# Kernel optimization log

Measured on AMD Instinct MI355X. Metric: run time of the kernel, lower is better.

## Reference

```python
import jax, jax.numpy as jnp
import numpy as np

N, E, D, H, LAYERS = 50000, 800000, 128, 8, 2
LRELU_ALPHA = 0.2


def _seg_softmax(logits, seg, n):
    # numerically stable softmax over edges grouped by destination node
    m = jax.ops.segment_max(logits, seg, num_segments=n)
    z = jnp.exp(logits - m[seg])
    s = jax.ops.segment_sum(z, seg, num_segments=n)
    return z / jnp.maximum(s[seg], 1e-16)


def _gat_layer(x, src, dst, W, a_src, a_dst, concat):
    # W: [H, Fin, F'], a_src/a_dst: [H, F']
    n = x.shape[0]
    outs = []
    for h in range(W.shape[0]):  # loop over heads to bound peak memory
        Wh = x @ W[h]                              # [N, F']
        es = Wh @ a_src[h]                         # [N]
        ed = Wh @ a_dst[h]                         # [N]
        e = jax.nn.leaky_relu(es[src] + ed[dst], LRELU_ALPHA)  # [E]
        att = _seg_softmax(e, dst, n)              # [E]
        out = jax.ops.segment_sum(att[:, None] * Wh[src], dst, num_segments=n)
        outs.append(out)
    if concat:
        return jax.nn.elu(jnp.concatenate(outs, axis=-1))  # [N, H*F']
    return jnp.mean(jnp.stack(outs, axis=0), axis=0)        # [N, F']


def _rel_gcn_layer(x, src, dst, w, W):
    # weighted-adjacency GCN with row (in-degree) normalization + ReLU
    n = x.shape[0]
    deg = jax.ops.segment_sum(w, dst, num_segments=n)
    norm = w / jnp.maximum(deg[dst], 1e-16)        # [E]
    h = x @ W                                      # [N, Dout]
    agg = jax.ops.segment_sum(norm[:, None] * h[src], dst, num_segments=n)
    return jax.nn.relu(agg)


def setup_inputs() -> dict:
    key = jax.random.key(0)
    ks = jax.random.split(key, 12)
    s = 1.0 / np.sqrt(D)
    return {
        "x": jax.random.normal(ks[0], (N, D), dtype=jnp.float32),
        "edge_index": jax.random.randint(ks[1], (2, E), 0, N, dtype=jnp.int64),
        "edge_weight": jax.random.uniform(ks[2], (E,), dtype=jnp.float32),
        "gat_W0": jax.random.normal(ks[3], (H, D, D // H), dtype=jnp.float32) * s,
        "gat_a0_src": jax.random.normal(ks[4], (H, D // H), dtype=jnp.float32) * s,
        "gat_a0_dst": jax.random.normal(ks[5], (H, D // H), dtype=jnp.float32) * s,
        "gat_W1": jax.random.normal(ks[6], (H, D, D), dtype=jnp.float32) * s,
        "gat_a1_src": jax.random.normal(ks[7], (H, D), dtype=jnp.float32) * s,
        "gat_a1_dst": jax.random.normal(ks[8], (H, D), dtype=jnp.float32) * s,
        "gcn_W0": jax.random.normal(ks[9], (D, D), dtype=jnp.float32) * s,
        "gcn_W1": jax.random.normal(ks[10], (D, D), dtype=jnp.float32) * s,
    }


def reference(x, edge_index, edge_weight, gat_W0, gat_a0_src, gat_a0_dst,
              gat_W1, gat_a1_src, gat_a1_dst, gcn_W0, gcn_W1):
    src, dst = edge_index[0], edge_index[1]
    gat_params = [(gat_W0, gat_a0_src, gat_a0_dst), (gat_W1, gat_a1_src, gat_a1_dst)]
    gcn_params = [gcn_W0, gcn_W1]
    x1, x2 = x, x  # dropout is identity in eval mode
    for i in range(LAYERS):
        W, a_s, a_d = gat_params[i]
        x1 = _gat_layer(x1, src, dst, W, a_s, a_d, concat=(i != LAYERS - 1))
        x2 = _rel_gcn_layer(x2, src, dst, edge_weight, gcn_params[i])
    # cat along new last dim then MaxPool1d(2) == elementwise max of branches
    return jnp.maximum(x1, x2)
```

## Files before the change

kernel.cpp:

```cpp
#include <hip/hip_runtime.h>

#define LRELU_ALPHA 0.2f

typedef __attribute__((ext_vector_type(8))) short short8;
typedef __attribute__((ext_vector_type(4))) float float4v;
typedef __attribute__((ext_vector_type(2))) float f32x2;

__device__ __forceinline__ unsigned short f2bf(float f) {
  union { float f; unsigned u; } x; x.f = f;
  unsigned r = (x.u + 0x7fff + ((x.u >> 16) & 1)) >> 16;
  return (unsigned short)r;
}
__device__ __forceinline__ float bflo(unsigned u) {
  union { unsigned u; float f; } x; x.u = u << 16; return x.f;
}
__device__ __forceinline__ float bfhi(unsigned u) {
  union { unsigned u; float f; } x; x.u = u & 0xffff0000u; return x.f;
}
__device__ __forceinline__ f32x2 bfpair(unsigned u) {
  return (f32x2){bflo(u), bfhi(u)};
}
__device__ __forceinline__ unsigned packbf(float a, float b) {
  return (unsigned)f2bf(a) | ((unsigned)f2bf(b) << 16);
}


__global__ __launch_bounds__(256) void k_count(const int* __restrict__ dst,
                                               int* __restrict__ cnt, int E) {
  int e = blockIdx.x * 256 + threadIdx.x;
  if (e < E) atomicAdd(&cnt[dst[e]], 1);
}

__global__ __launch_bounds__(1024) void k_scan1(const int* __restrict__ cnt,
                                                int* __restrict__ lscan,
                                                int* __restrict__ bsum, int N) {
  __shared__ int sm[1024];
  int t = threadIdx.x;
  int base = blockIdx.x * 1024;
  int v = (base + t < N) ? cnt[base + t] : 0;
  sm[t] = v;
  __syncthreads();
  for (int off = 1; off < 1024; off <<= 1) {
    int x = (t >= off) ? sm[t - off] : 0;
    __syncthreads();
    sm[t] += x;
    __syncthreads();
  }
  if (base + t < N) lscan[base + t] = sm[t] - v;
  if (t == 1023) bsum[blockIdx.x] = sm[1023];
}

__global__ __launch_bounds__(64) void k_scan2(int* __restrict__ bsum,
                                              int* __restrict__ rowptrN, int nb) {
  int t = threadIdx.x;
  int v = (t < nb) ? bsum[t] : 0;
  int orig = v;
  for (int off = 1; off < 64; off <<= 1) {
    int y = __shfl_up(v, off, 64);
    if (t >= off) v += y;
  }
  if (t < nb) bsum[t] = v - orig;
  if (t == 63) *rowptrN = v;
}

__global__ __launch_bounds__(1024) void k_scan3(int* __restrict__ rowptr,
                                                int* __restrict__ cur,
                                                const int* __restrict__ bsum, int N) {
  int i = blockIdx.x * 1024 + threadIdx.x;
  if (i < N) {
    int v = rowptr[i] + bsum[blockIdx.x];
    rowptr[i] = v;
    cur[i] = v;
  }
}

__global__ __launch_bounds__(256) void k_scatter(const int* __restrict__ src,
                                                 const int* __restrict__ dst,
                                                 const float* __restrict__ w,
                                                 const float* __restrict__ logit0,
                                                 int* __restrict__ cur,
                                                 uint2* __restrict__ edata,
                                                 unsigned short* __restrict__ pedge,
                                                 int E) {
  int base = (blockIdx.x * 256 + threadIdx.x) * 4;
  if (base >= E) return;
  int n = E - base; if (n > 4) n = 4;
  int ss[4], dd[4]; float ww[4];
  if (n == 4) {
    int4 s4 = *(const int4*)(src + base);
    int4 d4 = *(const int4*)(dst + base);
    float4 w4 = *(const float4*)(w + base);
    ss[0] = s4.x; ss[1] = s4.y; ss[2] = s4.z; ss[3] = s4.w;
    dd[0] = d4.x; dd[1] = d4.y; dd[2] = d4.z; dd[3] = d4.w;
    ww[0] = w4.x; ww[1] = w4.y; ww[2] = w4.z; ww[3] = w4.w;
  } else {
    for (int i = 0; i < n; ++i) { ss[i] = src[base + i]; dd[i] = dst[base + i]; ww[i] = w[base + i]; }
  }
  int pp[4];
#pragma unroll
  for (int i = 0; i < 4; ++i)
    if (i < n) pp[i] = atomicAdd(&cur[dd[i]], 1);
#pragma unroll
  for (int i = 0; i < 4; ++i) {
    if (i >= n) break;
    int s = ss[i], d = dd[i], p = pp[i];
    edata[p] = make_uint2((unsigned)s, __float_as_uint(ww[i]));
    float4 es0 = *(const float4*)(logit0 + (size_t)s * 16);
    float4 es1 = *(const float4*)(logit0 + (size_t)s * 16 + 4);
    float4 ed0 = *(const float4*)(logit0 + (size_t)d * 16 + 8);
    float4 ed1 = *(const float4*)(logit0 + (size_t)d * 16 + 12);
    float lg[8] = {es0.x + ed0.x, es0.y + ed0.y, es0.z + ed0.z, es0.w + ed0.w,
                   es1.x + ed1.x, es1.y + ed1.y, es1.z + ed1.z, es1.w + ed1.w};
    unsigned short o[8];
#pragma unroll
    for (int h = 0; h < 8; ++h) {
      float v = lg[h] > 0.f ? lg[h] : LRELU_ALPHA * lg[h];
      o[h] = f2bf(__expf(fminf(v, 80.f)));
    }
    ushort4 q0 = {o[0], o[1], o[2], o[3]};
    ushort4 q1 = {o[4], o[5], o[6], o[7]};
    *(ushort4*)(pedge + (size_t)p * 8) = q0;
    *(ushort4*)(pedge + (size_t)p * 8 + 4) = q1;
  }
}

__global__ __launch_bounds__(256) void k_pack(const float* __restrict__ W0,
                                              const float* __restrict__ a0s,
                                              const float* __restrict__ a0d,
                                              const float* __restrict__ W1,
                                              const float* __restrict__ a1s,
                                              const float* __restrict__ a1d,
                                              const float* __restrict__ gw0,
                                              const float* __restrict__ gw1,
                                              unsigned short* __restrict__ W0catT,
                                              float* __restrict__ logitW,
                                              unsigned short* __restrict__ gw1T,
                                              unsigned short* __restrict__ va1T,
                                              unsigned short* __restrict__ WstackT) {
  int idx = blockIdx.x * 256 + threadIdx.x;
  if (idx < 32768) {
    int n = idx >> 7, k = idx & 127;
    float v;
    if (n < 128) {
      int h = n >> 4, f = n & 15;
      v = W0[h * 2048 + k * 16 + f];
    } else {
      v = gw0[k * 128 + (n - 128)];
    }
    W0catT[idx] = f2bf(v);
  } else if (idx < 34816) {
    int j = idx - 32768;
    int k = j >> 4, c = j & 15;
    int h = (c < 8) ? c : c - 8;
    const float* a = (c < 8) ? a0s : a0d;
    float s = 0.f;
    for (int f = 0; f < 16; ++f) s += W0[h * 2048 + k * 16 + f] * a[h * 16 + f];
    logitW[j] = s;
  } else if (idx < 51200) {
    int j = idx - 34816;
    int n = j >> 7, k = j & 127;
    gw1T[j] = f2bf(gw1[k * 128 + n]);
  } else if (idx < 53248) {
    int j = idx - 51200;
    int c = j >> 7, k = j & 127;
    int h = c & 7;
    const float* a = (c < 8) ? a1s : a1d;
    float s = 0.f;
    for (int f = 0; f < 128; ++f) s += W1[h * 16384 + k * 128 + f] * a[h * 128 + f];
    va1T[j] = f2bf(s);
  } else if (idx < 184320) {
    int j = idx - 53248;
    int n = j >> 10, kk = j & 1023;
    int h = kk >> 7, k = kk & 127;
    WstackT[j] = f2bf(W1[h * 16384 + k * 128 + n] * 0.125f);
  }
}

__global__ __launch_bounds__(256) void k_prep(const float* __restrict__ x,
                                              const float* __restrict__ logitW,
                                              unsigned short* __restrict__ xb,
                                              float* __restrict__ logit0, int N) {
  __shared__ float sm[16][132];
  __shared__ float sw[2048];
  int t = threadIdx.x;
  int base = blockIdx.x * 16;
  int r = t >> 4, cc = (t & 15) * 8;
  const float* xr = x + (size_t)(base + r) * 128 + cc;
  float4 v0 = *(const float4*)xr;
  float4 v1 = *(const float4*)(xr + 4);
  ushort4 o0 = {f2bf(v0.x), f2bf(v0.y), f2bf(v0.z), f2bf(v0.w)};
  ushort4 o1 = {f2bf(v1.x), f2bf(v1.y), f2bf(v1.z), f2bf(v1.w)};
  *(ushort4*)(xb + (size_t)(base + r) * 128 + cc) = o0;
  *(ushort4*)(xb + (size_t)(base + r) * 128 + cc + 4) = o1;
  *(float4*)&sm[r][cc] = v0;
  *(float4*)&sm[r][cc + 4] = v1;
  *(float4*)&sw[t * 8] = *(const float4*)(logitW + t * 8);
  *(float4*)&sw[t * 8 + 4] = *(const float4*)(logitW + t * 8 + 4);
  __syncthreads();
  int c = t & 15;
  float acc = 0.f;
#pragma unroll
  for (int k = 0; k < 128; ++k) acc += sm[r][k] * sw[k * 16 + c];
  logit0[(size_t)(base + r) * 16 + c] = acc;
}

__global__ __launch_bounds__(256) void k_pedge(const float* __restrict__ logits,
                                               const uint2* __restrict__ edata,
                                               const int* __restrict__ rowptr,
                                               unsigned short* __restrict__ pedge,
                                               float* __restrict__ linv, int N) {
  int wave = threadIdx.x >> 6, lane = threadIdx.x & 63;
  int d = blockIdx.x * 4 + wave;
  if (d >= N) return;
  int j8 = lane >> 3, h = lane & 7;
  float edv = logits[(size_t)d * 16 + 8 + h];
  int beg = rowptr[d], end = rowptr[d + 1];
  float lsum = 0.f;
  for (int ii = beg + j8; ii < end; ii += 8) {
    unsigned s = edata[ii].x;
    float es = logits[(size_t)s * 16 + h];
    float lg = es + edv;
    lg = lg > 0.f ? lg : LRELU_ALPHA * lg;
    float p = __expf(fminf(lg, 80.f));
    lsum += p;
    pedge[(size_t)ii * 8 + h] = f2bf(p);
  }
  lsum += __shfl_xor(lsum, 8, 64);
  lsum += __shfl_xor(lsum, 16, 64);
  lsum += __shfl_xor(lsum, 32, 64);
  if (lane < 8) linv[(size_t)d * 8 + h] = lsum > 0.f ? 1.f / lsum : 0.f;
}

template <int NT, int OUT_BF16, int EPI>
__global__ __launch_bounds__(256) void k_mgemm(const unsigned short* __restrict__ A, int lda,
                                               const unsigned short* __restrict__ BT, int ldb,
                                               void* __restrict__ Cv, int ldc,
                                               const void* __restrict__ aux,
                                               int M, int Ncols, int K) {
  __shared__ unsigned short As[64][64];
  __shared__ unsigned short Bs[NT * 16][64];
  int tid = threadIdx.x;
  int w = tid >> 6, lane = tid & 63;
  int quad = lane >> 4, l16 = lane & 15;
  int row0 = blockIdx.x * 64;
  int c0 = blockIdx.y * (NT * 16);
  float4v acc[NT];
#pragma unroll
  for (int t = 0; t < NT; ++t) acc[t] = (float4v){0.f, 0.f, 0.f, 0.f};

  for (int k0 = 0; k0 < K; k0 += 64) {
    __syncthreads();
#pragma unroll
    for (int i = 0; i < 2; ++i) {
      int c = tid + i * 256;
      int r = c >> 3, kc = c & 7;
      uint4 v = {0u, 0u, 0u, 0u};
      int gr = row0 + r;
      if (gr < M) v = *(const uint4*)(A + (size_t)gr * lda + k0 + kc * 8);
      *(uint4*)(&As[r][(kc ^ (r & 7)) * 8]) = v;
    }
#pragma unroll
    for (int i = 0; i < (NT * 128 + 255) / 256; ++i) {
      int c = tid + i * 256;
      if (c < NT * 128) {
        int n = c >> 3, kc = c & 7;
        uint4 v = {0u, 0u, 0u, 0u};
        int gn = c0 + n;
        if (gn < Ncols) v = *(const uint4*)(BT + (size_t)gn * ldb + k0 + kc * 8);
        *(uint4*)(&Bs[n][(kc ^ (n & 7)) * 8]) = v;
      }
    }
    __syncthreads();
#pragma unroll
    for (int ks = 0; ks < 2; ++ks) {
      int m = w * 16 + l16;
      int ga = (ks * 4 + quad) ^ (m & 7);
      short8 a = *(const short8*)(&As[m][ga * 8]);
#pragma unroll
      for (int t = 0; t < NT; ++t) {
        int n = t * 16 + l16;
        int gb = (ks * 4 + quad) ^ (n & 7);
        short8 b = *(const short8*)(&Bs[n][gb * 8]);
        acc[t] = __builtin_amdgcn_mfma_f32_16x16x32_bf16(a, b, acc[t], 0, 0, 0);
      }
    }
  }
#pragma unroll
  for (int t = 0; t < NT; ++t) {
    int cc = c0 + t * 16 + l16;
    if (cc >= Ncols) continue;
#pragma unroll
    for (int i = 0; i < 4; ++i) {
      int rr = row0 + w * 16 + quad * 4 + i;
      if (rr >= M) continue;
      float v = acc[t][i];
      if (EPI == 1) {
        unsigned short us = ((const unsigned short*)aux)[(size_t)rr * ldc + cc];
        v = fmaxf(v, bflo((unsigned)us));
      }
      if (EPI == 2) {
        ((unsigned short*)Cv)[(size_t)rr * 256 + 4 * (cc >> 1) + 2 + (cc & 1)] = f2bf(v);
      } else if (EPI == 4) {
        if (cc < 128) {
          ((unsigned short*)Cv)[(size_t)rr * 128 + cc] = f2bf(v);
        } else {
          int enc = __builtin_amdgcn_cvt_pk_fp8_f32(v, v, 0, false);
          ((unsigned char*)aux)[(size_t)rr * 128 + (cc - 128)] = (unsigned char)(enc & 0xff);
        }
      } else if (OUT_BF16)
        ((unsigned short*)Cv)[(size_t)rr * ldc + cc] = f2bf(v);
      else
        ((float*)Cv)[(size_t)rr * ldc + cc] = v;
    }
  }
}

__global__ __launch_bounds__(256, 8) void k_agg0(const unsigned short* __restrict__ featg,
                                                 const unsigned char* __restrict__ featc,
                                                 const int* __restrict__ rowptr,
                                                 const uint2* __restrict__ edata,
                                                 const unsigned short* __restrict__ pedge,
                                                 unsigned short* __restrict__ x1c,
                                                 unsigned short* __restrict__ x2,
                                                 unsigned short* __restrict__ xh, int N) {
  __shared__ uint2 swl[4][64];
  __shared__ float pl[4][512];
  int wave = threadIdx.x >> 6, lane = threadIdx.x & 63;
  int head = lane >> 3;
  const unsigned* FG = (const unsigned*)featg + lane;
  const unsigned short* FC = (const unsigned short*)featc + lane;
  for (int d = blockIdx.x * 4 + wave; d < N; d += gridDim.x * 4) {
    int beg = rowptr[d], end = rowptr[d + 1], deg = end - beg;
    f32x2 aa = {0.f, 0.f}, ga = {0.f, 0.f};
    float l = 0.f, wsum = 0.f;
    for (int base = 0; base < deg; base += 64) {
      int idx = beg + base + lane;
      uint2 sv = make_uint2(0u, 0u);
      uint4 q = make_uint4(0u, 0u, 0u, 0u);
      if (idx < end) {
        sv = edata[idx];
        q = *(const uint4*)(pedge + (size_t)idx * 8);
      }
      swl[wave][lane] = sv;
      float4 pa = make_float4(bflo(q.x), bfhi(q.x), bflo(q.y), bfhi(q.y));
      float4 pb = make_float4(bflo(q.z), bfhi(q.z), bflo(q.w), bfhi(q.w));
      *(float4*)&pl[wave][lane * 8] = pa;
      *(float4*)&pl[wave][lane * 8 + 4] = pb;
      int ng = deg - base; if (ng > 64) ng = 64;
      int t = 0;
      for (; t + 4 <= ng; t += 4) {
        uint2 s0 = swl[wave][t], s1 = swl[wave][t + 1];
        uint2 s2 = swl[wave][t + 2], s3 = swl[wave][t + 3];
        unsigned g0 = FG[(size_t)s0.x * 64];
        unsigned g1 = FG[(size_t)s1.x * 64];
        unsigned g2 = FG[(size_t)s2.x * 64];
        unsigned g3 = FG[(size_t)s3.x * 64];
        unsigned c0 = (unsigned)FC[(size_t)s0.x * 64];
        unsigned c1 = (unsigned)FC[(size_t)s1.x * 64];
        unsigned c2 = (unsigned)FC[(size_t)s2.x * 64];
        unsigned c3 = (unsigned)FC[(size_t)s3.x * 64];
        float p0 = pl[wave][t * 8 + head];
        float p1 = pl[wave][t * 8 + 8 + head];
        float p2 = pl[wave][t * 8 + 16 + head];
        float p3 = pl[wave][t * 8 + 24 + head];
        float w0 = __uint_as_float(s0.y), w1 = __uint_as_float(s1.y);
        float w2 = __uint_as_float(s2.y), w3 = __uint_as_float(s3.y);
        aa += bfpair(g0) * p0; ga += __builtin_amdgcn_cvt_pk_f32_fp8(c0, false) * w0;
        l += p0; wsum += w0;
        aa += bfpair(g1) * p1; ga += __builtin_amdgcn_cvt_pk_f32_fp8(c1, false) * w1;
        l += p1; wsum += w1;
        aa += bfpair(g2) * p2; ga += __builtin_amdgcn_cvt_pk_f32_fp8(c2, false) * w2;
        l += p2; wsum += w2;
        aa += bfpair(g3) * p3; ga += __builtin_amdgcn_cvt_pk_f32_fp8(c3, false) * w3;
        l += p3; wsum += w3;
      }
      for (; t < ng; ++t) {
        uint2 s0 = swl[wave][t];
        unsigned g0 = FG[(size_t)s0.x * 64];
        unsigned c0 = (unsigned)FC[(size_t)s0.x * 64];
        float p0 = pl[wave][t * 8 + head];
        float w0 = __uint_as_float(s0.y);
        aa += bfpair(g0) * p0; ga += __builtin_amdgcn_cvt_pk_f32_fp8(c0, false) * w0;
        l += p0; wsum += w0;
      }
    }
    float inv = l > 0.f ? 1.f / l : 0.f;
    float v0 = aa.x * inv, v1 = aa.y * inv;
    v0 = v0 > 0.f ? v0 : __expf(v0) - 1.f;
    v1 = v1 > 0.f ? v1 : __expf(v1) - 1.f;
    unsigned p0 = packbf(v0, v1);
    ((unsigned*)x1c)[(size_t)d * 64 + lane] = p0;
    ((unsigned*)xh)[(size_t)d * 128 + 2 * lane] = p0;
    float ginv = 1.f / fmaxf(wsum, 1e-16f);
    ((unsigned*)x2)[(size_t)d * 64 + lane] =
        packbf(fmaxf(ga.x * ginv, 0.f), fmaxf(ga.y * ginv, 0.f));
  }
}

__global__ __launch_bounds__(256, 8) void k_agg1(const unsigned short* __restrict__ xh,
                                                 const int* __restrict__ rowptr,
                                                 const uint2* __restrict__ edata,
                                                 const unsigned short* __restrict__ pedge,
                                                 const float* __restrict__ linv,
                                                 unsigned short* __restrict__ aggbuf,
                                                 unsigned short* __restrict__ x2f, int N) {
  __shared__ uint2 swl[4][64];
  __shared__ float pl[4][512];
  int wave = threadIdx.x >> 6, lane = threadIdx.x & 63;
  const uint2* X2 = (const uint2*)xh + lane;
  for (int d = blockIdx.x * 4 + wave; d < N; d += gridDim.x * 4) {
    int beg = rowptr[d], end = rowptr[d + 1], deg = end - beg;
    f32x2 axp[8] = {};
    f32x2 gp = {0.f, 0.f};
    float wsum = 0.f;
#define EDGE1(uu, ss, tt)                                    \
  {                                                          \
    float4 pv0 = *(const float4*)&pl[wave][(tt) * 8];        \
    float4 pv1 = *(const float4*)&pl[wave][(tt) * 8 + 4];    \
    float wj = __uint_as_float((ss).y);                      \
    f32x2 xA = bfpair((uu).x), hA = bfpair((uu).y);          \
    axp[0] += xA * pv0.x; axp[1] += xA * pv0.y;              \
    axp[2] += xA * pv0.z; axp[3] += xA * pv0.w;              \
    axp[4] += xA * pv1.x; axp[5] += xA * pv1.y;              \
    axp[6] += xA * pv1.z; axp[7] += xA * pv1.w;              \
    gp += hA * wj; wsum += wj;                               \
  }
    for (int base = 0; base < deg; base += 64) {
      int idx = beg + base + lane;
      uint2 sv = make_uint2(0u, 0u);
      uint4 q = make_uint4(0u, 0u, 0u, 0u);
      if (idx < end) {
        sv = edata[idx];
        q = *(const uint4*)(pedge + (size_t)idx * 8);
      }
      swl[wave][lane] = sv;
      float4 pa = make_float4(bflo(q.x), bfhi(q.x), bflo(q.y), bfhi(q.y));
      float4 pb = make_float4(bflo(q.z), bfhi(q.z), bflo(q.w), bfhi(q.w));
      *(float4*)&pl[wave][lane * 8] = pa;
      *(float4*)&pl[wave][lane * 8 + 4] = pb;
      int ng = deg - base; if (ng > 64) ng = 64;
      int t = 0;
      for (; t + 4 <= ng; t += 4) {
        uint2 s0 = swl[wave][t], s1 = swl[wave][t + 1];
        uint2 s2 = swl[wave][t + 2], s3 = swl[wave][t + 3];
        uint2 u0 = X2[(size_t)s0.x * 64];
        uint2 u1 = X2[(size_t)s1.x * 64];
        uint2 u2 = X2[(size_t)s2.x * 64];
        uint2 u3 = X2[(size_t)s3.x * 64];
        EDGE1(u0, s0, t)
        EDGE1(u1, s1, t + 1)
        EDGE1(u2, s2, t + 2)
        EDGE1(u3, s3, t + 3)
      }
      for (; t < ng; ++t) {
        uint2 s0 = swl[wave][t];
        uint2 u0 = X2[(size_t)s0.x * 64];
        EDGE1(u0, s0, t)
      }
    }
#undef EDGE1
    float4 i0 = *(const float4*)(linv + (size_t)d * 8);
    float4 i1 = *(const float4*)(linv + (size_t)d * 8 + 4);
    unsigned* ab = (unsigned*)aggbuf + (size_t)d * 512 + lane;
    ab[0]   = packbf(axp[0].x * i0.x, axp[0].y * i0.x);
    ab[64]  = packbf(axp[1].x * i0.y, axp[1].y * i0.y);
    ab[128] = packbf(axp[2].x * i0.z, axp[2].y * i0.z);
    ab[192] = packbf(axp[3].x * i0.w, axp[3].y * i0.w);
    ab[256] = packbf(axp[4].x * i1.x, axp[4].y * i1.x);
    ab[320] = packbf(axp[5].x * i1.y, axp[5].y * i1.y);
    ab[384] = packbf(axp[6].x * i1.z, axp[6].y * i1.z);
    ab[448] = packbf(axp[7].x * i1.w, axp[7].y * i1.w);
    float ginv = 1.f / fmaxf(wsum, 1e-16f);
    ((unsigned*)x2f)[(size_t)d * 64 + lane] =
        packbf(fmaxf(gp.x * ginv, 0.f), fmaxf(gp.y * ginv, 0.f));
  }
}


extern "C" void kernel_launch(void* const* d_in, const int* in_sizes, int n_in,
                              void* d_out, int out_size, void* d_ws, size_t ws_size,
                              hipStream_t stream) {
  const float* x   = (const float*)d_in[0];
  const int*   ei  = (const int*)d_in[1];
  const float* ew  = (const float*)d_in[2];
  const float* W0  = (const float*)d_in[3];
  const float* a0s = (const float*)d_in[4];
  const float* a0d = (const float*)d_in[5];
  const float* W1  = (const float*)d_in[6];
  const float* a1s = (const float*)d_in[7];
  const float* a1d = (const float*)d_in[8];
  const float* gw0 = (const float*)d_in[9];
  const float* gw1 = (const float*)d_in[10];
  float* out = (float*)d_out;

  const int N = in_sizes[0] / 128;
  const int E = in_sizes[1] / 2;
  const int* src = ei;
  const int* dst = ei + E;

  char* p = (char*)d_ws;
  auto carve = [&](size_t bytes) {
    void* r = (void*)p;
    p += (bytes + 255) & ~(size_t)255;
    return r;
  };
  int*   cnt    = (int*)carve((size_t)N * 4);
  int*   rowptr = (int*)carve((size_t)(N + 1) * 4);
  int*   cur    = (int*)carve((size_t)N * 4);
  int*   bsum   = (int*)carve(256 * 4);
  uint2* edata  = (uint2*)carve((size_t)E * 8);
  unsigned short* W0catT  = (unsigned short*)carve(32768 * 2);
  float*          logitW  = (float*)carve(2048 * 4);
  unsigned short* gw1T    = (unsigned short*)carve(16384 * 2);
  unsigned short* va1T    = (unsigned short*)carve(2048 * 2);
  unsigned short* WstackT = (unsigned short*)carve(131072 * 2);
  unsigned short* x2   = (unsigned short*)carve((size_t)N * 128 * 2);
  float*          esed = (float*)carve((size_t)N * 16 * 4);
  unsigned short* xh   = (unsigned short*)carve((size_t)N * 256 * 2);
  unsigned short* pedge = (unsigned short*)carve((size_t)E * 8 * 2);
  float*          linv1 = (float*)carve((size_t)N * 8 * 4);
  size_t ph1 = ((size_t)N * 128 * 2 + 255) & ~(size_t)255;
  size_t ph2 = ph1 + (((size_t)N * 128 * 2 + 255) & ~(size_t)255);
  size_t ph3 = ph2 + (((size_t)N * 128 + 255) & ~(size_t)255);
  size_t ph4 = ph3 + (((size_t)N * 16 * 4 + 255) & ~(size_t)255);
  size_t scratch_sz = (size_t)N * 1024 * 2;
  if (ph4 > scratch_sz) scratch_sz = ph4;
  char* scratch = (char*)carve(scratch_sz);
  unsigned short* xb     = (unsigned short*)scratch;
  unsigned short* x1c    = (unsigned short*)scratch;
  unsigned short* featg  = (unsigned short*)(scratch + ph1);
  unsigned char*  featc  = (unsigned char*)(scratch + ph2);
  float*          logit0 = (float*)(scratch + ph3);
  unsigned short* aggbuf = (unsigned short*)scratch;
  unsigned short* x2f    = x2;

  int gE = (E + 255) / 256;
  int gE4 = ((E + 3) / 4 + 255) / 256;
  int nb = (N + 1023) / 1024;
  int gM = (N + 63) / 64;
  int gD = (N + 3) / 4;
  int gA = gD < 2048 ? gD : 2048;

  hipMemsetAsync(cnt, 0, (size_t)N * 4, stream);
  k_count<<<gE, 256, 0, stream>>>(dst, cnt, E);
  k_scan1<<<nb, 1024, 0, stream>>>(cnt, rowptr, bsum, N);
  k_scan2<<<1, 64, 0, stream>>>(bsum, rowptr + N, nb);
  k_scan3<<<nb, 1024, 0, stream>>>(rowptr, cur, bsum, N);

  k_pack<<<(184320 + 255) / 256, 256, 0, stream>>>(W0, a0s, a0d, W1, a1s, a1d, gw0,
                                                   gw1, W0catT, logitW, gw1T, va1T,
                                                   WstackT);
  k_prep<<<(N + 15) / 16, 256, 0, stream>>>(x, logitW, xb, logit0, N);

  k_scatter<<<gE4, 256, 0, stream>>>(src, dst, ew, logit0, cur, edata, pedge, E);

  k_mgemm<8, 1, 4><<<dim3(gM, 2), 256, 0, stream>>>(xb, 128, W0catT, 128, featg, 128,
                                                    featc, N, 256, 128);
  k_agg0<<<gA, 256, 0, stream>>>(featg, featc, rowptr, edata, pedge, x1c, x2, xh, N);

  k_mgemm<1, 0, 0><<<dim3(gM, 1), 256, 0, stream>>>(x1c, 128, va1T, 128, esed, 16,
                                                    nullptr, N, 16, 128);
  k_mgemm<8, 1, 2><<<dim3(gM, 1), 256, 0, stream>>>(x2, 128, gw1T, 128, xh, 256,
                                                    nullptr, N, 128, 128);

  k_pedge<<<gD, 256, 0, stream>>>(esed, edata, rowptr, pedge, linv1, N);

  k_agg1<<<gA, 256, 0, stream>>>(xh, rowptr, edata, pedge, linv1, aggbuf, x2f, N);

  k_mgemm<8, 0, 1><<<dim3(gM, 1), 256, 0, stream>>>(aggbuf, 1024, WstackT, 1024, out,
                                                    128, x2f, N, 128, 1024);
}
```

Baseline: 458.6 us.

## Compute edge attention on the fly in aggregation kernels and reorder GCN layer two

Removes the precomputed bf16 per-edge attention buffer and the separate k_pedge kernel. Both aggregation kernels now gather source logits per edge, apply leaky-ReLU and exp themselves, and reduce the softmax denominator in-register. The second GCN layer is reordered to aggregate first and then apply the weight matrix, with ReLU moved into the GEMM epilogue. This cuts edge-sized writes and reads plus one launch, at the cost of extra random logit gathers and exp work inside the aggregation loops, and an in-place GEMM on x2a.

```diff
diff --git a/kernel.cpp b/kernel.cpp
--- a/kernel.cpp
+++ b/kernel.cpp
@@ -77,11 +77,8 @@
 __global__ __launch_bounds__(256) void k_scatter(const int* __restrict__ src,
                                                  const int* __restrict__ dst,
                                                  const float* __restrict__ w,
-                                                 const float* __restrict__ logit0,
                                                  int* __restrict__ cur,
-                                                 uint2* __restrict__ edata,
-                                                 unsigned short* __restrict__ pedge,
-                                                 int E) {
+                                                 uint2* __restrict__ edata, int E) {
   int base = (blockIdx.x * 256 + threadIdx.x) * 4;
   if (base >= E) return;
   int n = E - base; if (n > 4) n = 4;
@@ -101,27 +98,8 @@
   for (int i = 0; i < 4; ++i)
     if (i < n) pp[i] = atomicAdd(&cur[dd[i]], 1);
 #pragma unroll
-  for (int i = 0; i < 4; ++i) {
-    if (i >= n) break;
-    int s = ss[i], d = dd[i], p = pp[i];
-    edata[p] = make_uint2((unsigned)s, __float_as_uint(ww[i]));
-    float4 es0 = *(const float4*)(logit0 + (size_t)s * 16);
-    float4 es1 = *(const float4*)(logit0 + (size_t)s * 16 + 4);
-    float4 ed0 = *(const float4*)(logit0 + (size_t)d * 16 + 8);
-    float4 ed1 = *(const float4*)(logit0 + (size_t)d * 16 + 12);
-    float lg[8] = {es0.x + ed0.x, es0.y + ed0.y, es0.z + ed0.z, es0.w + ed0.w,
-                   es1.x + ed1.x, es1.y + ed1.y, es1.z + ed1.z, es1.w + ed1.w};
-    unsigned short o[8];
-#pragma unroll
-    for (int h = 0; h < 8; ++h) {
-      float v = lg[h] > 0.f ? lg[h] : LRELU_ALPHA * lg[h];
-      o[h] = f2bf(__expf(fminf(v, 80.f)));
-    }
-    ushort4 q0 = {o[0], o[1], o[2], o[3]};
-    ushort4 q1 = {o[4], o[5], o[6], o[7]};
-    *(ushort4*)(pedge + (size_t)p * 8) = q0;
-    *(ushort4*)(pedge + (size_t)p * 8 + 4) = q1;
-  }
+  for (int i = 0; i < 4; ++i)
+    if (i < n) edata[pp[i]] = make_uint2((unsigned)ss[i], __float_as_uint(ww[i]));
 }
 
 __global__ __launch_bounds__(256) void k_pack(const float* __restrict__ W0,
@@ -204,33 +182,6 @@
   logit0[(size_t)(base + r) * 16 + c] = acc;
 }
 
-__global__ __launch_bounds__(256) void k_pedge(const float* __restrict__ logits,
-                                               const uint2* __restrict__ edata,
-                                               const int* __restrict__ rowptr,
-                                               unsigned short* __restrict__ pedge,
-                                               float* __restrict__ linv, int N) {
-  int wave = threadIdx.x >> 6, lane = threadIdx.x & 63;
-  int d = blockIdx.x * 4 + wave;
-  if (d >= N) return;
-  int j8 = lane >> 3, h = lane & 7;
-  float edv = logits[(size_t)d * 16 + 8 + h];
-  int beg = rowptr[d], end = rowptr[d + 1];
-  float lsum = 0.f;
-  for (int ii = beg + j8; ii < end; ii += 8) {
-    unsigned s = edata[ii].x;
-    float es = logits[(size_t)s * 16 + h];
-    float lg = es + edv;
-    lg = lg > 0.f ? lg : LRELU_ALPHA * lg;
-    float p = __expf(fminf(lg, 80.f));
-    lsum += p;
-    pedge[(size_t)ii * 8 + h] = f2bf(p);
-  }
-  lsum += __shfl_xor(lsum, 8, 64);
-  lsum += __shfl_xor(lsum, 16, 64);
-  lsum += __shfl_xor(lsum, 32, 64);
-  if (lane < 8) linv[(size_t)d * 8 + h] = lsum > 0.f ? 1.f / lsum : 0.f;
-}
-
 template <int NT, int OUT_BF16, int EPI>
 __global__ __launch_bounds__(256) void k_mgemm(const unsigned short* __restrict__ A, int lda,
                                                const unsigned short* __restrict__ BT, int ldb,
@@ -298,9 +249,8 @@
         unsigned short us = ((const unsigned short*)aux)[(size_t)rr * ldc + cc];
         v = fmaxf(v, bflo((unsigned)us));
       }
-      if (EPI == 2) {
-        ((unsigned short*)Cv)[(size_t)rr * 256 + 4 * (cc >> 1) + 2 + (cc & 1)] = f2bf(v);
-      } else if (EPI == 4) {
+      if (EPI == 5) v = fmaxf(v, 0.f);
+      if (EPI == 4) {
         if (cc < 128) {
           ((unsigned short*)Cv)[(size_t)rr * 128 + cc] = f2bf(v);
         } else {
@@ -319,34 +269,38 @@
                                                  const unsigned char* __restrict__ featc,
                                                  const int* __restrict__ rowptr,
                                                  const uint2* __restrict__ edata,
-                                                 const unsigned short* __restrict__ pedge,
+                                                 const float* __restrict__ logit0,
                                                  unsigned short* __restrict__ x1c,
-                                                 unsigned short* __restrict__ x2,
-                                                 unsigned short* __restrict__ xh, int N) {
+                                                 unsigned short* __restrict__ x2, int N) {
   __shared__ uint2 swl[4][64];
   __shared__ float pl[4][512];
+  __shared__ __align__(16) float lnv[4][8];
   int wave = threadIdx.x >> 6, lane = threadIdx.x & 63;
-  int head = lane >> 3;
+  int head = lane >> 3, h8 = lane & 7, e8 = lane >> 3;
   const unsigned* FG = (const unsigned*)featg + lane;
   const unsigned short* FC = (const unsigned short*)featc + lane;
   for (int d = blockIdx.x * 4 + wave; d < N; d += gridDim.x * 4) {
     int beg = rowptr[d], end = rowptr[d + 1], deg = end - beg;
+    float edv = logit0[(size_t)d * 16 + 8 + h8];
     f32x2 aa = {0.f, 0.f}, ga = {0.f, 0.f};
-    float l = 0.f, wsum = 0.f;
+    float lsum = 0.f, wsum = 0.f;
     for (int base = 0; base < deg; base += 64) {
       int idx = beg + base + lane;
       uint2 sv = make_uint2(0u, 0u);
-      uint4 q = make_uint4(0u, 0u, 0u, 0u);
-      if (idx < end) {
-        sv = edata[idx];
-        q = *(const uint4*)(pedge + (size_t)idx * 8);
-      }
+      if (idx < end) sv = edata[idx];
       swl[wave][lane] = sv;
-      float4 pa = make_float4(bflo(q.x), bfhi(q.x), bflo(q.y), bfhi(q.y));
-      float4 pb = make_float4(bflo(q.z), bfhi(q.z), bflo(q.w), bfhi(q.w));
-      *(float4*)&pl[wave][lane * 8] = pa;
-      *(float4*)&pl[wave][lane * 8 + 4] = pb;
       int ng = deg - base; if (ng > 64) ng = 64;
+#pragma unroll
+      for (int j = 0; j < 8; ++j) {
+        int e = j * 8 + e8;
+        unsigned s = swl[wave][e].x;
+        float es = logit0[(size_t)s * 16 + h8];
+        float lg = es + edv;
+        lg = lg > 0.f ? lg : LRELU_ALPHA * lg;
+        float p = (e < ng) ? __expf(fminf(lg, 80.f)) : 0.f;
+        pl[wave][j * 64 + lane] = p;
+        lsum += p;
+      }
       int t = 0;
       for (; t + 4 <= ng; t += 4) {
         uint2 s0 = swl[wave][t], s1 = swl[wave][t + 1];
@@ -365,14 +319,10 @@
         float p3 = pl[wave][t * 8 + 24 + head];
         float w0 = __uint_as_float(s0.y), w1 = __uint_as_float(s1.y);
         float w2 = __uint_as_float(s2.y), w3 = __uint_as_float(s3.y);
-        aa += bfpair(g0) * p0; ga += __builtin_amdgcn_cvt_pk_f32_fp8(c0, false) * w0;
-        l += p0; wsum += w0;
-        aa += bfpair(g1) * p1; ga += __builtin_amdgcn_cvt_pk_f32_fp8(c1, false) * w1;
-        l += p1; wsum += w1;
-        aa += bfpair(g2) * p2; ga += __builtin_amdgcn_cvt_pk_f32_fp8(c2, false) * w2;
-        l += p2; wsum += w2;
-        aa += bfpair(g3) * p3; ga += __builtin_amdgcn_cvt_pk_f32_fp8(c3, false) * w3;
-        l += p3; wsum += w3;
+        aa += bfpair(g0) * p0; ga += __builtin_amdgcn_cvt_pk_f32_fp8(c0, false) * w0; wsum += w0;
+        aa += bfpair(g1) * p1; ga += __builtin_amdgcn_cvt_pk_f32_fp8(c1, false) * w1; wsum += w1;
+        aa += bfpair(g2) * p2; ga += __builtin_amdgcn_cvt_pk_f32_fp8(c2, false) * w2; wsum += w2;
+        aa += bfpair(g3) * p3; ga += __builtin_amdgcn_cvt_pk_f32_fp8(c3, false) * w3; wsum += w3;
       }
       for (; t < ng; ++t) {
         uint2 s0 = swl[wave][t];
@@ -380,45 +330,50 @@
         unsigned c0 = (unsigned)FC[(size_t)s0.x * 64];
         float p0 = pl[wave][t * 8 + head];
         float w0 = __uint_as_float(s0.y);
-        aa += bfpair(g0) * p0; ga += __builtin_amdgcn_cvt_pk_f32_fp8(c0, false) * w0;
-        l += p0; wsum += w0;
-      }
-    }
-    float inv = l > 0.f ? 1.f / l : 0.f;
+        aa += bfpair(g0) * p0; ga += __builtin_amdgcn_cvt_pk_f32_fp8(c0, false) * w0; wsum += w0;
+      }
+    }
+    lsum += __shfl_xor(lsum, 8, 64);
+    lsum += __shfl_xor(lsum, 16, 64);
+    lsum += __shfl_xor(lsum, 32, 64);
+    if (lane < 8) lnv[wave][lane] = lsum > 0.f ? 1.f / lsum : 0.f;
+    float inv = lnv[wave][head];
     float v0 = aa.x * inv, v1 = aa.y * inv;
     v0 = v0 > 0.f ? v0 : __expf(v0) - 1.f;
     v1 = v1 > 0.f ? v1 : __expf(v1) - 1.f;
-    unsigned p0 = packbf(v0, v1);
-    ((unsigned*)x1c)[(size_t)d * 64 + lane] = p0;
-    ((unsigned*)xh)[(size_t)d * 128 + 2 * lane] = p0;
+    ((unsigned*)x1c)[(size_t)d * 64 + lane] = packbf(v0, v1);
     float ginv = 1.f / fmaxf(wsum, 1e-16f);
     ((unsigned*)x2)[(size_t)d * 64 + lane] =
         packbf(fmaxf(ga.x * ginv, 0.f), fmaxf(ga.y * ginv, 0.f));
   }
 }
 
-__global__ __launch_bounds__(256, 8) void k_agg1(const unsigned short* __restrict__ xh,
+__global__ __launch_bounds__(256, 8) void k_agg1(const unsigned short* __restrict__ x1t,
+                                                 const unsigned short* __restrict__ x2t,
+                                                 const float* __restrict__ esed,
                                                  const int* __restrict__ rowptr,
                                                  const uint2* __restrict__ edata,
-                                                 const unsigned short* __restrict__ pedge,
-                                                 const float* __restrict__ linv,
                                                  unsigned short* __restrict__ aggbuf,
-                                                 unsigned short* __restrict__ x2f, int N) {
+                                                 unsigned short* __restrict__ x2a, int N) {
   __shared__ uint2 swl[4][64];
   __shared__ float pl[4][512];
+  __shared__ __align__(16) float lnv[4][8];
   int wave = threadIdx.x >> 6, lane = threadIdx.x & 63;
-  const uint2* X2 = (const uint2*)xh + lane;
+  int h8 = lane & 7, e8 = lane >> 3;
+  const unsigned* X1 = (const unsigned*)x1t + lane;
+  const unsigned* XG = (const unsigned*)x2t + lane;
   for (int d = blockIdx.x * 4 + wave; d < N; d += gridDim.x * 4) {
     int beg = rowptr[d], end = rowptr[d + 1], deg = end - beg;
+    float edv = esed[(size_t)d * 16 + 8 + h8];
     f32x2 axp[8] = {};
     f32x2 gp = {0.f, 0.f};
-    float wsum = 0.f;
-#define EDGE1(uu, ss, tt)                                    \
+    float lsum = 0.f, wsum = 0.f;
+#define EDGE1(u1, u2, ss, tt)                                \
   {                                                          \
     float4 pv0 = *(const float4*)&pl[wave][(tt) * 8];        \
     float4 pv1 = *(const float4*)&pl[wave][(tt) * 8 + 4];    \
     float wj = __uint_as_float((ss).y);                      \
-    f32x2 xA = bfpair((uu).x), hA = bfpair((uu).y);          \
+    f32x2 xA = bfpair(u1), hA = bfpair(u2);                  \
     axp[0] += xA * pv0.x; axp[1] += xA * pv0.y;              \
     axp[2] += xA * pv0.z; axp[3] += xA * pv0.w;              \
     axp[4] += xA * pv1.x; axp[5] += xA * pv1.y;              \
@@ -428,39 +383,46 @@
     for (int base = 0; base < deg; base += 64) {
       int idx = beg + base + lane;
       uint2 sv = make_uint2(0u, 0u);
-      uint4 q = make_uint4(0u, 0u, 0u, 0u);
-      if (idx < end) {
-        sv = edata[idx];
-        q = *(const uint4*)(pedge + (size_t)idx * 8);
-      }
+      if (idx < end) sv = edata[idx];
       swl[wave][lane] = sv;
-      float4 pa = make_float4(bflo(q.x), bfhi(q.x), bflo(q.y), bfhi(q.y));
-      float4 pb = make_float4(bflo(q.z), bfhi(q.z), bflo(q.w), bfhi(q.w));
-      *(float4*)&pl[wave][lane * 8] = pa;
-      *(float4*)&pl[wave][lane * 8 + 4] = pb;
       int ng = deg - base; if (ng > 64) ng = 64;
+#pragma unroll
+      for (int j = 0; j < 8; ++j) {
+        int e = j * 8 + e8;
+        unsigned s = swl[wave][e].x;
+        float es = esed[(size_t)s * 16 + h8];
+        float lg = es + edv;
+        lg = lg > 0.f ? lg : LRELU_ALPHA * lg;
+        float p = (e < ng) ? __expf(fminf(lg, 80.f)) : 0.f;
+        pl[wave][j * 64 + lane] = p;
+        lsum += p;
+      }
       int t = 0;
       for (; t + 4 <= ng; t += 4) {
         uint2 s0 = swl[wave][t], s1 = swl[wave][t + 1];
         uint2 s2 = swl[wave][t + 2], s3 = swl[wave][t + 3];
-        uint2 u0 = X2[(size_t)s0.x * 64];
-        uint2 u1 = X2[(size_t)s1.x * 64];
-        uint2 u2 = X2[(size_t)s2.x * 64];
-        uint2 u3 = X2[(size_t)s3.x * 64];
-        EDGE1(u0, s0, t)
-        EDGE1(u1, s1, t + 1)
-        EDGE1(u2, s2, t + 2)
-        EDGE1(u3, s3, t + 3)
+        unsigned a0 = X1[(size_t)s0.x * 64], b0 = XG[(size_t)s0.x * 64];
+        unsigned a1 = X1[(size_t)s1.x * 64], b1 = XG[(size_t)s1.x * 64];
+        unsigned a2 = X1[(size_t)s2.x * 64], b2 = XG[(size_t)s2.x * 64];
+        unsigned a3 = X1[(size_t)s3.x * 64], b3 = XG[(size_t)s3.x * 64];
+        EDGE1(a0, b0, s0, t)
+        EDGE1(a1, b1, s1, t + 1)
+        EDGE1(a2, b2, s2, t + 2)
+        EDGE1(a3, b3, s3, t + 3)
       }
       for (; t < ng; ++t) {
         uint2 s0 = swl[wave][t];
-        uint2 u0 = X2[(size_t)s0.x * 64];
-        EDGE1(u0, s0, t)
+        unsigned a0 = X1[(size_t)s0.x * 64], b0 = XG[(size_t)s0.x * 64];
+        EDGE1(a0, b0, s0, t)
       }
     }
 #undef EDGE1
-    float4 i0 = *(const float4*)(linv + (size_t)d * 8);
-    float4 i1 = *(const float4*)(linv + (size_t)d * 8 + 4);
+    lsum += __shfl_xor(lsum, 8, 64);
+    lsum += __shfl_xor(lsum, 16, 64);
+    lsum += __shfl_xor(lsum, 32, 64);
+    if (lane < 8) lnv[wave][lane] = lsum > 0.f ? 1.f / lsum : 0.f;
+    const float4* lp = (const float4*)lnv[wave];
+    float4 i0 = lp[0], i1 = lp[1];
     unsigned* ab = (unsigned*)aggbuf + (size_t)d * 512 + lane;
     ab[0]   = packbf(axp[0].x * i0.x, axp[0].y * i0.x);
     ab[64]  = packbf(axp[1].x * i0.y, axp[1].y * i0.y);
@@ -471,8 +433,7 @@
     ab[384] = packbf(axp[6].x * i1.z, axp[6].y * i1.z);
     ab[448] = packbf(axp[7].x * i1.w, axp[7].y * i1.w);
     float ginv = 1.f / fmaxf(wsum, 1e-16f);
-    ((unsigned*)x2f)[(size_t)d * 64 + lane] =
-        packbf(fmaxf(gp.x * ginv, 0.f), fmaxf(gp.y * ginv, 0.f));
+    ((unsigned*)x2a)[(size_t)d * 64 + lane] = packbf(gp.x * ginv, gp.y * ginv);
   }
 }
 
@@ -516,9 +477,8 @@
   unsigned short* WstackT = (unsigned short*)carve(131072 * 2);
   unsigned short* x2   = (unsigned short*)carve((size_t)N * 128 * 2);
   float*          esed = (float*)carve((size_t)N * 16 * 4);
-  unsigned short* xh   = (unsigned short*)carve((size_t)N * 256 * 2);
-  unsigned short* pedge = (unsigned short*)carve((size_t)E * 8 * 2);
-  float*          linv1 = (float*)carve((size_t)N * 8 * 4);
+  unsigned short* x1ct = (unsigned short*)carve((size_t)N * 128 * 2);
+  unsigned short* x2a  = (unsigned short*)carve((size_t)N * 128 * 2);
   size_t ph1 = ((size_t)N * 128 * 2 + 255) & ~(size_t)255;
   size_t ph2 = ph1 + (((size_t)N * 128 * 2 + 255) & ~(size_t)255);
   size_t ph3 = ph2 + (((size_t)N * 128 + 255) & ~(size_t)255);
@@ -527,12 +487,10 @@
   if (ph4 > scratch_sz) scratch_sz = ph4;
   char* scratch = (char*)carve(scratch_sz);
   unsigned short* xb     = (unsigned short*)scratch;
-  unsigned short* x1c    = (unsigned short*)scratch;
   unsigned short* featg  = (unsigned short*)(scratch + ph1);
   unsigned char*  featc  = (unsigned char*)(scratch + ph2);
   float*          logit0 = (float*)(scratch + ph3);
   unsigned short* aggbuf = (unsigned short*)scratch;
-  unsigned short* x2f    = x2;
 
   int gE = (E + 255) / 256;
   int gE4 = ((E + 3) / 4 + 255) / 256;
@@ -547,26 +505,25 @@
   k_scan2<<<1, 64, 0, stream>>>(bsum, rowptr + N, nb);
   k_scan3<<<nb, 1024, 0, stream>>>(rowptr, cur, bsum, N);
 
+  k_scatter<<<gE4, 256, 0, stream>>>(src, dst, ew, cur, edata, E);
+
   k_pack<<<(184320 + 255) / 256, 256, 0, stream>>>(W0, a0s, a0d, W1, a1s, a1d, gw0,
                                                    gw1, W0catT, logitW, gw1T, va1T,
                                                    WstackT);
   k_prep<<<(N + 15) / 16, 256, 0, stream>>>(x, logitW, xb, logit0, N);
 
-  k_scatter<<<gE4, 256, 0, stream>>>(src, dst, ew, logit0, cur, edata, pedge, E);
-
   k_mgemm<8, 1, 4><<<dim3(gM, 2), 256, 0, stream>>>(xb, 128, W0catT, 128, featg, 128,
                                                     featc, N, 256, 128);
-  k_agg0<<<gA, 256, 0, stream>>>(featg, featc, rowptr, edata, pedge, x1c, x2, xh, N);
-
-  k_mgemm<1, 0, 0><<<dim3(gM, 1), 256, 0, stream>>>(x1c, 128, va1T, 128, esed, 16,
+  k_agg0<<<gA, 256, 0, stream>>>(featg, featc, rowptr, edata, logit0, x1ct, x2, N);
+
+  k_mgemm<1, 0, 0><<<dim3(gM, 1), 256, 0, stream>>>(x1ct, 128, va1T, 128, esed, 16,
                                                     nullptr, N, 16, 128);
-  k_mgemm<8, 1, 2><<<dim3(gM, 1), 256, 0, stream>>>(x2, 128, gw1T, 128, xh, 256,
+
+  k_agg1<<<gA, 256, 0, stream>>>(x1ct, x2, esed, rowptr, edata, aggbuf, x2a, N);
+
+  k_mgemm<8, 1, 5><<<dim3(gM, 1), 256, 0, stream>>>(x2a, 128, gw1T, 128, x2a, 128,
                                                     nullptr, N, 128, 128);
 
-  k_pedge<<<gD, 256, 0, stream>>>(esed, edata, rowptr, pedge, linv1, N);
-
-  k_agg1<<<gA, 256, 0, stream>>>(xh, rowptr, edata, pedge, linv1, aggbuf, x2f, N);
-
   k_mgemm<8, 0, 1><<<dim3(gM, 1), 256, 0, stream>>>(aggbuf, 1024, WstackT, 1024, out,
-                                                    128, x2f, N, 128, 1024);
-}
+                                                    128, x2a, N, 128, 1024);
+}
```

Measured after the change: 494.6 us. +7.8%, slower.
